# Optimization experiments

Measured on AMD Instinct MI355X. Metric: run time of the kernel, lower is better.

Reference implementation:

```python
import jax, jax.numpy as jnp
import numpy as np

B, N, HS, NH = 32, 256, 768, 32
D = HS // NH  # 24


def setup_inputs() -> dict:
    key = jax.random.key(0)
    ks = jax.random.split(key, 20)
    s = 0.02
    inp = {
        "hidden_states": jax.random.normal(ks[0], (B, N, HS), jnp.float32),
        "attention_bias": jax.random.normal(ks[1], (B, NH, N, N), jnp.float32),
        "delta_pos": jax.random.normal(ks[2], (B, N, N, 3), jnp.float32),
        "attention_mask": jnp.ones((B, N), jnp.float32),
        "Wi": jax.random.normal(ks[3], (HS, HS), jnp.float32) * s,
        "bi": jnp.zeros((HS,), jnp.float32),
        "Wq": jax.random.normal(ks[4], (HS, HS), jnp.float32) * s,
        "bq": jnp.zeros((HS,), jnp.float32),
        "Wk": jax.random.normal(ks[5], (HS, HS), jnp.float32) * s,
        "bk": jnp.zeros((HS,), jnp.float32),
        "Wv": jax.random.normal(ks[6], (HS, HS), jnp.float32) * s,
        "bv": jnp.zeros((HS,), jnp.float32),
        "Wf1": jax.random.normal(ks[7], (1, HS), jnp.float32) * s,
        "bf1": jnp.zeros((1,), jnp.float32),
        "Wf2": jax.random.normal(ks[8], (1, HS), jnp.float32) * s,
        "bf2": jnp.zeros((1,), jnp.float32),
        "Wf3": jax.random.normal(ks[9], (1, HS), jnp.float32) * s,
        "bf3": jnp.zeros((1,), jnp.float32),
    }
    return inp


def reference(hidden_states, attention_bias, delta_pos, attention_mask,
              Wi, bi, Wq, bq, Wk, bk, Wv, bv, Wf1, bf1, Wf2, bf2, Wf3, bf3):
    b, n, hs = hidden_states.shape
    nh = NH
    d = hs // nh
    denoise_scaling = d ** (-0.5)
    scale = np.sqrt(denoise_scaling).astype(np.float32)

    # mask: (B,N) -> additive (B,1,1,N)
    neg = ((1.0 - attention_mask) * -100000.0)[:, None, None, :]

    h = jax.nn.gelu(hidden_states @ Wi.T + bi, approximate=False)
    q = (h @ Wq.T + bq).reshape(b, n, nh, d).transpose(0, 2, 1, 3) * scale
    k = (h @ Wk.T + bk).reshape(b, n, nh, d).transpose(0, 2, 1, 3) * scale
    v = (h @ Wv.T + bv).reshape(b, n, nh, d).transpose(0, 2, 1, 3)

    scores = jnp.einsum('bhid,bhjd->bhij', q, k) + attention_bias + neg
    probs = jax.nn.softmax(scores, axis=-1)  # dropout = identity at eval

    # x[b,i,c,h,d] = sum_j probs[b,h,i,j] * delta_pos[b,i,j,c] * v[b,h,j,d]
    x = jnp.einsum('bhij,bijc,bhjd->bichd', probs, delta_pos, v)
    x = x.reshape(b, n, 3, hs)

    f1 = x[:, :, 0, :] @ Wf1.T + bf1  # (B,N,1)
    f2 = x[:, :, 1, :] @ Wf2.T + bf2
    f3 = x[:, :, 2, :] @ Wf3.T + bf3
    return jnp.concatenate([f1, f2, f3], axis=-1).astype(jnp.float32)
```

## Files before the change

### kernel.cpp

```cpp
#include <hip/hip_runtime.h>
#include <hip/hip_fp16.h>

#define B_  32
#define N_  256
#define HS_ 768
#define NH_ 32
#define D_  24
#define M_  (B_*N_)
#define QKVN 2304

typedef unsigned short us8 __attribute__((ext_vector_type(8)));
typedef _Float16 f16x8 __attribute__((ext_vector_type(8)));
typedef float f32x4 __attribute__((ext_vector_type(4)));

__device__ __forceinline__ unsigned short f2h(float x){
  return __half_as_ushort(__float2half(x));
}
__device__ __forceinline__ float h2f(unsigned short u){
  return __half2float(__ushort_as_half(u));
}
__device__ __forceinline__ void gload16(const void* g, void* l){
  __builtin_amdgcn_global_load_lds(
      (const __attribute__((address_space(1))) void*)g,
      (__attribute__((address_space(3))) void*)l, 16, 0, 0);
}

__global__ __launch_bounds__(256) void cvt_kernel(const float* __restrict__ in,
                                                  unsigned short* __restrict__ out, int n4){
  int i = blockIdx.x*256 + threadIdx.x;
  if (i >= n4) return;
  float4 v = ((const float4*)in)[i];
  ushort4 o;
  o.x = f2h(v.x); o.y = f2h(v.y); o.z = f2h(v.z); o.w = f2h(v.w);
  ((ushort4*)out)[i] = o;
}

__global__ __launch_bounds__(256) void gemm128_kernel(
    const unsigned short* __restrict__ A, const unsigned short* __restrict__ W,
    const float* __restrict__ b0, const float* __restrict__ b1, const float* __restrict__ b2,
    unsigned short* __restrict__ C, int M, int N, int K, int dogelu)
{
  __shared__ unsigned short As[128*64];
  __shared__ unsigned short Bs[128*64];
  int gswz = blockIdx.x;
  int chunkg = gridDim.x >> 3;
  int bid = (gswz & 7)*chunkg + (gswz >> 3);
  int tid = threadIdx.x;
  int nT = N >> 7;
  int tm = bid / nT;
  int tn = bid - tm*nT;
  int which = (tn << 7) / 768;
  const float* bp = (which == 0) ? b0 : (which == 1) ? b1 : b2;
  bp -= which * 768;
  int wave = tid >> 6, lane = tid & 63;
  int wm = (wave >> 1) << 6;
  int wn = (wave & 1) << 6;
  int fr = lane & 15;
  int g  = lane >> 4;

  size_t aoff[4], woff[4];
  int ldsb[4];
#pragma unroll
  for (int s4 = 0; s4 < 4; s4++){
    int ob = s4*4096 + tid*16;
    int r  = ob >> 7;
    int p  = (ob >> 4) & 7;
    int l  = p ^ (r & 7);
    aoff[s4] = ((size_t)(tm*128 + r)*K)*2 + l*16;
    woff[s4] = ((size_t)(tn*128 + r)*K)*2 + l*16;
    ldsb[s4] = s4*4096 + wave*1024;
  }
  const char* Ab = (const char*)A;
  const char* Wb = (const char*)W;
  char* AsB = (char*)As;
  char* BsB = (char*)Bs;

  f32x4 acc[4][4];
#pragma unroll
  for (int m = 0; m < 4; m++)
#pragma unroll
    for (int n = 0; n < 4; n++) acc[m][n] = (f32x4){0.f,0.f,0.f,0.f};

  for (int k0 = 0; k0 < K; k0 += 64){
    size_t kb = (size_t)k0*2;
#pragma unroll
    for (int s4 = 0; s4 < 4; s4++) gload16(Ab + aoff[s4] + kb, AsB + ldsb[s4]);
#pragma unroll
    for (int s4 = 0; s4 < 4; s4++) gload16(Wb + woff[s4] + kb, BsB + ldsb[s4]);
    __syncthreads();

    f16x8 af[4], bf[4];
#pragma unroll
    for (int m = 0; m < 4; m++){
      int row = wm + m*16 + fr;
      af[m] = __builtin_bit_cast(f16x8, *(const us8*)(AsB + row*128 + ((g ^ (row & 7))*16)));
    }
#pragma unroll
    for (int n = 0; n < 4; n++){
      int row = wn + n*16 + fr;
      bf[n] = __builtin_bit_cast(f16x8, *(const us8*)(BsB + row*128 + ((g ^ (row & 7))*16)));
    }
#pragma unroll
    for (int m = 0; m < 4; m++)
#pragma unroll
      for (int n = 0; n < 4; n++)
        acc[m][n] = __builtin_amdgcn_mfma_f32_16x16x32_f16(af[m], bf[n], acc[m][n], 0, 0, 0);

#pragma unroll
    for (int m = 0; m < 4; m++){
      int row = wm + m*16 + fr;
      af[m] = __builtin_bit_cast(f16x8, *(const us8*)(AsB + row*128 + (((g+4) ^ (row & 7))*16)));
    }
#pragma unroll
    for (int n = 0; n < 4; n++){
      int row = wn + n*16 + fr;
      bf[n] = __builtin_bit_cast(f16x8, *(const us8*)(BsB + row*128 + (((g+4) ^ (row & 7))*16)));
    }
#pragma unroll
    for (int m = 0; m < 4; m++)
#pragma unroll
      for (int n = 0; n < 4; n++)
        acc[m][n] = __builtin_amdgcn_mfma_f32_16x16x32_f16(af[m], bf[n], acc[m][n], 0, 0, 0);
    __syncthreads();
  }

#pragma unroll
  for (int n = 0; n < 4; n++){
    int col = tn*128 + wn + n*16 + fr;
    float bv = bp[col];
#pragma unroll
    for (int m = 0; m < 4; m++){
      int row = tm*128 + wm + m*16 + g*4;
#pragma unroll
      for (int q = 0; q < 4; q++){
        float v = acc[m][n][q] + bv;
        if (dogelu) v = 0.5f*v*(1.0f + erff(v*0.70710678118654752f));
        C[(size_t)(row + q)*N + col] = f2h(v);
      }
    }
  }
}

__global__ __launch_bounds__(256) void prep_kernel(
    const unsigned short* __restrict__ qkv, const float* __restrict__ mask,
    const float* __restrict__ Wf1, const float* __restrict__ Wf2, const float* __restrict__ Wf3,
    float* __restrict__ uarr,
    float* __restrict__ negv)
{
  int bh = blockIdx.x;
  int h = bh & 31, b = bh >> 5;
  int j = threadIdx.x;
  const unsigned short* vr = qkv + (size_t)(b*N_ + j)*QKVN + 1536 + h*D_;
  us8 v0 = *(const us8*)(vr);
  us8 v1 = *(const us8*)(vr + 8);
  us8 v2 = *(const us8*)(vr + 16);
  const float* w1 = Wf1 + h*D_;
  const float* w2 = Wf2 + h*D_;
  const float* w3 = Wf3 + h*D_;
  float u0 = 0.f, u1 = 0.f, u2 = 0.f;
#pragma unroll
  for (int e = 0; e < 8; e++){
    float va = h2f(v0[e]), vb2 = h2f(v1[e]), vc = h2f(v2[e]);
    u0 += va*w1[e] + vb2*w1[8+e] + vc*w1[16+e];
    u1 += va*w2[e] + vb2*w2[8+e] + vc*w2[16+e];
    u2 += va*w3[e] + vb2*w3[8+e] + vc*w3[16+e];
  }
  float* ub = uarr + (size_t)bh*3*N_;
  ub[j] = u0; ub[N_ + j] = u1; ub[2*N_ + j] = u2;
  if (h == 0) negv[b*N_ + j] = (1.0f - mask[b*N_ + j]) * -100000.0f;
}

#define SCALE 0.20412414523193154f
#define INVSCALE 4.898979485566356f
#define M0 16.0f
#define BUFSZ 32768
__global__ __launch_bounds__(256, 2) void attn_kernel(
    const unsigned short* __restrict__ qkv,
    const float* __restrict__ bias,
    const float* __restrict__ uarr, const float* __restrict__ negv,
    const float* __restrict__ dp,
    const float* __restrict__ bf1, const float* __restrict__ bf2, const float* __restrict__ bf3,
    float* __restrict__ out)
{
  int gswz = blockIdx.x;
  int lin = (gswz & 7)*64 + (gswz >> 3);
  int b = lin >> 4, chunk = lin & 15;
  int i0 = chunk*16;
  int t = threadIdx.x;
  int wave = t >> 6, lane = t & 63;
  int ch = wave, fr = lane & 15, g = lane >> 4;

  __shared__ __align__(16) char smem[72192];
  char* zp     = smem + 65536;
  float* negsF = (float*)(smem + 69632);
  float* redv  = (float*)(smem + 70656);
  float4* redvE= (float4*)(smem + 71168);

  int bsrc[4];
#pragma unroll
  for (int r = 0; r < 4; r++){
    int a = r*4096 + t*16;
    int row = a >> 10;
    int pc = (a >> 4) & 63;
    int lc = pc ^ (row & 7);
    bsrc[r] = row*1024 + lc*16;
  }
  const char* bb0 = (const char*)bias + (((size_t)(b*32)*256 + i0)*256)*4;
  const char* kq0 = (const char*)(qkv + (size_t)(b*N_ + t)*QKVN + 768);
  const char* ub0 = (const char*)(uarr + (size_t)(b*32)*768);
  const char* uqsrc0;
  int uqstep;
  if (t < 192){ uqsrc0 = ub0 + t*16; uqstep = 3072; }
  else if (t < 240){
    int rr = (t-192)/3, cc = (t-192)%3;
    uqsrc0 = (const char*)(qkv + (size_t)(b*N_ + i0 + rr)*QKVN) + cc*16;
    uqstep = 48;
  } else { uqsrc0 = ub0; uqstep = 3072; }

  #define ISSUE(hh, nx) do { \
    const char* _bB = bb0 + (size_t)(hh)*262144; \
    _Pragma("unroll") \
    for (int _r = 0; _r < 4; _r++) gload16(_bB + bsrc[_r], (nx) + _r*4096 + wave*1024); \
    const char* _kB = kq0 + (hh)*48; \
    _Pragma("unroll") \
    for (int _c = 0; _c < 3; _c++) gload16(_kB + _c*16, (nx) + 16384 + _c*4096 + wave*1024); \
    gload16(uqsrc0 + (size_t)(hh)*uqstep, (nx) + 28672 + wave*1024); \
  } while(0)

  ISSUE(0, smem);
  float4 dpre[12];
  {
    const float* dpb = dp + (size_t)(b*N_ + i0 + fr)*768;
#pragma unroll
    for (int jt = 0; jt < 4; jt++){
      const float4* q4 = (const float4*)(dpb + (ch*64 + jt*16 + g*4)*3);
      dpre[jt*3+0] = q4[0]; dpre[jt*3+1] = q4[1]; dpre[jt*3+2] = q4[2];
    }
  }
  *(us8*)(zp + t*16) = (us8){0,0,0,0,0,0,0,0};
  negsF[t] = negv[b*N_ + t];
  asm volatile("s_waitcnt lgkmcnt(0)" ::: "memory");

  f32x4 G[4][3];
#pragma unroll
  for (int jt = 0; jt < 4; jt++)
#pragma unroll
    for (int c = 0; c < 3; c++) G[jt][c] = (f32x4){0.f,0.f,0.f,0.f};

  int swz = (fr & 7) << 4;

#pragma unroll 1
  for (int h = 0; h < 32; h++){
    int par = h & 1;
    char* bufb = smem + par*BUFSZ;
    char* nxb  = smem + (par^1)*BUFSZ;
    if (h < 31){
      ISSUE(h+1, nxb);
      asm volatile("s_waitcnt vmcnt(8)" ::: "memory");
    } else {
      asm volatile("s_waitcnt vmcnt(0)" ::: "memory");
    }
    __builtin_amdgcn_s_barrier();

    const char* qa = (g < 3) ? (bufb + 28672 + 3072 + fr*48 + g*16) : (zp + fr*16);
    f16x8 qf = __builtin_bit_cast(f16x8, *(const us8*)qa);

    float rowsum = 0.f;
    f32x4 tt[4][3];
#pragma unroll
    for (int jt = 0; jt < 4; jt++){
      int j0 = ch*64 + jt*16 + g*4;
      float4 bv = *(const float4*)(bufb + fr*1024 + ((j0*4) ^ swz));
      float4 nv = *(const float4*)&negsF[j0];
      f32x4 cin;
      cin[0] = (bv.x + nv.x)*INVSCALE;
      cin[1] = (bv.y + nv.y)*INVSCALE;
      cin[2] = (bv.z + nv.z)*INVSCALE;
      cin[3] = (bv.w + nv.w)*INVSCALE;
      int krow = ch*64 + jt*16 + fr;
      const char* ka = (g < 3) ? (bufb + 16384 + g*4096 + krow*16) : (zp + krow*16);
      f16x8 kf = __builtin_bit_cast(f16x8, *(const us8*)ka);
      f32x4 sv = __builtin_amdgcn_mfma_f32_16x16x32_f16(kf, qf, cin, 0, 0, 0);
      f32x4 p;
      p[0] = __expf(fmaf(sv[0], SCALE, -M0));
      p[1] = __expf(fmaf(sv[1], SCALE, -M0));
      p[2] = __expf(fmaf(sv[2], SCALE, -M0));
      p[3] = __expf(fmaf(sv[3], SCALE, -M0));
      rowsum += p[0] + p[1] + p[2] + p[3];
      const char* ub = bufb + 28672;
#pragma unroll
      for (int c = 0; c < 3; c++){
        f32x4 uv = __builtin_bit_cast(f32x4, *(const float4*)(ub + c*1024 + j0*4));
        tt[jt][c] = p * uv;
      }
    }
    rowsum += __shfl_xor(rowsum, 16);
    rowsum += __shfl_xor(rowsum, 32);
    if (lane < 16) redv[(par*16 + fr)*4 + ch] = rowsum;
    asm volatile("s_waitcnt lgkmcnt(0)" ::: "memory");
    __builtin_amdgcn_s_barrier();
    float4 rv = *(const float4*)&redv[(par*16 + fr)*4];
    float rs = 1.0f / (rv.x + rv.y + rv.z + rv.w);
#pragma unroll
    for (int jt = 0; jt < 4; jt++)
#pragma unroll
      for (int c = 0; c < 3; c++){
        G[jt][c][0] = fmaf(rs, tt[jt][c][0], G[jt][c][0]);
        G[jt][c][1] = fmaf(rs, tt[jt][c][1], G[jt][c][1]);
        G[jt][c][2] = fmaf(rs, tt[jt][c][2], G[jt][c][2]);
        G[jt][c][3] = fmaf(rs, tt[jt][c][3], G[jt][c][3]);
      }
  }
  #undef ISSUE

  float a0 = 0.f, a1 = 0.f, a2 = 0.f;
#pragma unroll
  for (int jt = 0; jt < 4; jt++){
    float4 d0 = dpre[jt*3], d1 = dpre[jt*3+1], d2 = dpre[jt*3+2];
    a0 += G[jt][0][0]*d0.x + G[jt][0][1]*d0.w + G[jt][0][2]*d1.z + G[jt][0][3]*d2.y;
    a1 += G[jt][1][0]*d0.y + G[jt][1][1]*d1.x + G[jt][1][2]*d1.w + G[jt][1][3]*d2.z;
    a2 += G[jt][2][0]*d0.z + G[jt][2][1]*d1.y + G[jt][2][2]*d2.x + G[jt][2][3]*d2.w;
  }
  a0 += __shfl_xor(a0, 16); a0 += __shfl_xor(a0, 32);
  a1 += __shfl_xor(a1, 16); a1 += __shfl_xor(a1, 32);
  a2 += __shfl_xor(a2, 16); a2 += __shfl_xor(a2, 32);
  if (lane < 16) redvE[fr*4 + ch] = make_float4(a0, a1, a2, 0.f);
  asm volatile("s_waitcnt lgkmcnt(0)" ::: "memory");
  __builtin_amdgcn_s_barrier();
  if (t < 16){
    float4 e0 = redvE[t*4+0], e1 = redvE[t*4+1], e2 = redvE[t*4+2], e3 = redvE[t*4+3];
    float* op = out + (size_t)(b*N_ + i0 + t)*3;
    op[0] = e0.x + e1.x + e2.x + e3.x + bf1[0];
    op[1] = e0.y + e1.y + e2.y + e3.y + bf2[0];
    op[2] = e0.z + e1.z + e2.z + e3.z + bf3[0];
  }
}

extern "C" void kernel_launch(void* const* d_in, const int* in_sizes, int n_in,
                              void* d_out, int out_size, void* d_ws, size_t ws_size,
                              hipStream_t stream)
{
  const float* X    = (const float*)d_in[0];
  const float* bias = (const float*)d_in[1];
  const float* dp   = (const float*)d_in[2];
  const float* mask = (const float*)d_in[3];
  const float* Wi   = (const float*)d_in[4];
  const float* bi   = (const float*)d_in[5];
  const float* Wq   = (const float*)d_in[6];
  const float* bq   = (const float*)d_in[7];
  const float* Wk   = (const float*)d_in[8];
  const float* bk   = (const float*)d_in[9];
  const float* Wv   = (const float*)d_in[10];
  const float* bv   = (const float*)d_in[11];
  const float* Wf1  = (const float*)d_in[12];
  const float* bf1  = (const float*)d_in[13];
  const float* Wf2  = (const float*)d_in[14];
  const float* bf2  = (const float*)d_in[15];
  const float* Wf3  = (const float*)d_in[16];
  const float* bf3  = (const float*)d_in[17];
  float* out = (float*)d_out;

  unsigned short* xb   = (unsigned short*)d_ws;
  unsigned short* wib  = xb   + (size_t)M_*HS_;
  unsigned short* wqb  = wib  + (size_t)HS_*HS_;
  unsigned short* wkb  = wqb  + (size_t)HS_*HS_;
  unsigned short* wvb  = wkb  + (size_t)HS_*HS_;
  unsigned short* hb   = wvb  + (size_t)HS_*HS_;
  unsigned short* qkvb = hb   + (size_t)M_*HS_;
  float* uarr  = (float*)(qkvb + (size_t)M_*QKVN);
  float* negv  = uarr + (size_t)B_*NH_*3*N_;

  {
    int n4 = M_*HS_/4;
    cvt_kernel<<<n4/256, 256, 0, stream>>>(X, xb, n4);
    int w4 = HS_*HS_/4;
    cvt_kernel<<<w4/256, 256, 0, stream>>>(Wi, wib, w4);
    cvt_kernel<<<w4/256, 256, 0, stream>>>(Wq, wqb, w4);
    cvt_kernel<<<w4/256, 256, 0, stream>>>(Wk, wkb, w4);
    cvt_kernel<<<w4/256, 256, 0, stream>>>(Wv, wvb, w4);
  }

  gemm128_kernel<<<(M_/128)*(HS_/128), 256, 0, stream>>>(xb, wib, bi, bi, bi, hb, M_, HS_, HS_, 1);
  gemm128_kernel<<<(M_/128)*(QKVN/128), 256, 0, stream>>>(hb, wqb, bq, bk, bv, qkvb, M_, QKVN, HS_, 0);

  prep_kernel<<<B_*NH_, 256, 0, stream>>>(qkvb, mask, Wf1, Wf2, Wf3, uarr, negv);

  attn_kernel<<<B_*16, 256, 0, stream>>>(qkvb, bias, uarr, negv, dp,
                                         bf1, bf2, bf3, out);
}
```

Baseline: 181.4 us.

## Deepen bias prefetch to four LDS slots and load K/Q directly into registers

Restructures the attention kernel's per-head pipeline. Bias tiles now go through a 4-slot LDS ring prefetched three heads ahead, while u values use a separate double buffer. K and Q fragments are loaded straight from global memory into ping-ponged registers one head ahead instead of staging them in LDS. The mask values are kept in registers and the delta_pos loads are moved to after the loop to free registers. The aim is to hide more of the bias streaming latency and cut LDS traffic, at the cost of more LDS (75 KB, which still allows 2 blocks per CU) and more in-flight registers.

```diff
diff --git a/kernel.cpp b/kernel.cpp
--- a/kernel.cpp
+++ b/kernel.cpp
@@ -173,7 +173,6 @@
 #define SCALE 0.20412414523193154f
 #define INVSCALE 4.898979485566356f
 #define M0 16.0f
-#define BUFSZ 32768
 __global__ __launch_bounds__(256, 2) void attn_kernel(
     const unsigned short* __restrict__ qkv,
     const float* __restrict__ bias,
@@ -190,11 +189,9 @@
   int wave = t >> 6, lane = t & 63;
   int ch = wave, fr = lane & 15, g = lane >> 4;
 
-  __shared__ __align__(16) char smem[72192];
-  char* zp     = smem + 65536;
-  float* negsF = (float*)(smem + 69632);
-  float* redv  = (float*)(smem + 70656);
-  float4* redvE= (float4*)(smem + 71168);
+  __shared__ __align__(16) char smem[75264];
+  float*  redv  = (float*)(smem + 73728);
+  float4* redvE = (float4*)(smem + 74240);
 
   int bsrc[4];
 #pragma unroll
@@ -206,40 +203,47 @@
     bsrc[r] = row*1024 + lc*16;
   }
   const char* bb0 = (const char*)bias + (((size_t)(b*32)*256 + i0)*256)*4;
-  const char* kq0 = (const char*)(qkv + (size_t)(b*N_ + t)*QKVN + 768);
   const char* ub0 = (const char*)(uarr + (size_t)(b*32)*768);
-  const char* uqsrc0;
-  int uqstep;
-  if (t < 192){ uqsrc0 = ub0 + t*16; uqstep = 3072; }
-  else if (t < 240){
-    int rr = (t-192)/3, cc = (t-192)%3;
-    uqsrc0 = (const char*)(qkv + (size_t)(b*N_ + i0 + rr)*QKVN) + cc*16;
-    uqstep = 48;
-  } else { uqsrc0 = ub0; uqstep = 3072; }
-
-  #define ISSUE(hh, nx) do { \
-    const char* _bB = bb0 + (size_t)(hh)*262144; \
+  int uoff = (t*16 <= 3056) ? t*16 : 3056;
+  const char* kqB = (const char*)qkv;
+  size_t krow[4];
+#pragma unroll
+  for (int jt = 0; jt < 4; jt++)
+    krow[jt] = ((size_t)(b*N_ + ch*64 + jt*16 + fr))*4608 + 1536 + g*16;
+  size_t qrow = ((size_t)(b*N_ + i0 + fr))*4608 + g*16;
+
+  #define ISSUE_BIAS(hh, slot) do { \
+    const char* _s = bb0 + (size_t)(hh)*262144; \
+    char* _d = smem + (slot)*16384; \
     _Pragma("unroll") \
-    for (int _r = 0; _r < 4; _r++) gload16(_bB + bsrc[_r], (nx) + _r*4096 + wave*1024); \
-    const char* _kB = kq0 + (hh)*48; \
+    for (int _r = 0; _r < 4; _r++) gload16(_s + bsrc[_r], _d + _r*4096 + wave*1024); \
+  } while(0)
+  #define ISSUE_U(hh, par) \
+    gload16(ub0 + (size_t)(hh)*3072 + uoff, smem + 65536 + (par)*4096 + wave*1024)
+  #define ISSUE_KQ(hh, kn, qn) do { \
     _Pragma("unroll") \
-    for (int _c = 0; _c < 3; _c++) gload16(_kB + _c*16, (nx) + 16384 + _c*4096 + wave*1024); \
-    gload16(uqsrc0 + (size_t)(hh)*uqstep, (nx) + 28672 + wave*1024); \
+    for (int _jt = 0; _jt < 4; _jt++) \
+      kn[_jt] = __builtin_bit_cast(f16x8, *(const us8*)(kqB + krow[_jt] + (hh)*48)); \
+    qn = __builtin_bit_cast(f16x8, *(const us8*)(kqB + qrow + (hh)*48)); \
   } while(0)
 
-  ISSUE(0, smem);
-  float4 dpre[12];
-  {
-    const float* dpb = dp + (size_t)(b*N_ + i0 + fr)*768;
-#pragma unroll
-    for (int jt = 0; jt < 4; jt++){
-      const float4* q4 = (const float4*)(dpb + (ch*64 + jt*16 + g*4)*3);
-      dpre[jt*3+0] = q4[0]; dpre[jt*3+1] = q4[1]; dpre[jt*3+2] = q4[2];
-    }
-  }
-  *(us8*)(zp + t*16) = (us8){0,0,0,0,0,0,0,0};
-  negsF[t] = negv[b*N_ + t];
-  asm volatile("s_waitcnt lgkmcnt(0)" ::: "memory");
+  float4 nv[4];
+#pragma unroll
+  for (int jt = 0; jt < 4; jt++)
+    nv[jt] = *(const float4*)(negv + b*N_ + ch*64 + jt*16 + g*4);
+
+  f16x8 kA[4], kB[4], qA, qB;
+  f16x8 zero8 = __builtin_bit_cast(f16x8, (us8){0,0,0,0,0,0,0,0});
+
+  ISSUE_BIAS(0, 0);
+  ISSUE_U(0, 0);
+  ISSUE_KQ(0, kA, qA);
+  __builtin_amdgcn_sched_barrier(0);
+  ISSUE_BIAS(1, 1);
+  ISSUE_BIAS(2, 2);
+  __builtin_amdgcn_sched_barrier(0);
+  asm volatile("s_waitcnt vmcnt(8)" ::: "memory");
+  __builtin_amdgcn_s_barrier();
 
   f32x4 G[4][3];
 #pragma unroll
@@ -249,48 +253,43 @@
 
   int swz = (fr & 7) << 4;
 
-#pragma unroll 1
-  for (int h = 0; h < 32; h++){
+  auto body = [&](int h, f16x8 (&kc)[4], f16x8 &qc, f16x8 (&kn)[4], f16x8 &qn)
+      __attribute__((always_inline)) {
+    int hu = (h + 1) & 31;
+    ISSUE_U(hu, (h + 1) & 1);
+    ISSUE_KQ(hu, kn, qn);
+    __builtin_amdgcn_sched_barrier(0);
+    ISSUE_BIAS((h + 3) & 31, (h + 3) & 3);
+    __builtin_amdgcn_sched_barrier(0);
+    asm volatile("s_waitcnt vmcnt(14)" ::: "memory");
+    __builtin_amdgcn_s_barrier();
+
+    const char* bslot = smem + (h & 3)*16384;
+    const char* ubuf  = smem + 65536 + (h & 1)*4096;
+    f16x8 qf = (g < 3) ? qc : zero8;
     int par = h & 1;
-    char* bufb = smem + par*BUFSZ;
-    char* nxb  = smem + (par^1)*BUFSZ;
-    if (h < 31){
-      ISSUE(h+1, nxb);
-      asm volatile("s_waitcnt vmcnt(8)" ::: "memory");
-    } else {
-      asm volatile("s_waitcnt vmcnt(0)" ::: "memory");
-    }
-    __builtin_amdgcn_s_barrier();
-
-    const char* qa = (g < 3) ? (bufb + 28672 + 3072 + fr*48 + g*16) : (zp + fr*16);
-    f16x8 qf = __builtin_bit_cast(f16x8, *(const us8*)qa);
 
     float rowsum = 0.f;
     f32x4 tt[4][3];
 #pragma unroll
     for (int jt = 0; jt < 4; jt++){
       int j0 = ch*64 + jt*16 + g*4;
-      float4 bv = *(const float4*)(bufb + fr*1024 + ((j0*4) ^ swz));
-      float4 nv = *(const float4*)&negsF[j0];
+      float4 bv = *(const float4*)(bslot + fr*1024 + ((j0*4) ^ swz));
       f32x4 cin;
-      cin[0] = (bv.x + nv.x)*INVSCALE;
-      cin[1] = (bv.y + nv.y)*INVSCALE;
-      cin[2] = (bv.z + nv.z)*INVSCALE;
-      cin[3] = (bv.w + nv.w)*INVSCALE;
-      int krow = ch*64 + jt*16 + fr;
-      const char* ka = (g < 3) ? (bufb + 16384 + g*4096 + krow*16) : (zp + krow*16);
-      f16x8 kf = __builtin_bit_cast(f16x8, *(const us8*)ka);
-      f32x4 sv = __builtin_amdgcn_mfma_f32_16x16x32_f16(kf, qf, cin, 0, 0, 0);
+      cin[0] = (bv.x + nv[jt].x)*INVSCALE;
+      cin[1] = (bv.y + nv[jt].y)*INVSCALE;
+      cin[2] = (bv.z + nv[jt].z)*INVSCALE;
+      cin[3] = (bv.w + nv[jt].w)*INVSCALE;
+      f32x4 sv = __builtin_amdgcn_mfma_f32_16x16x32_f16(kc[jt], qf, cin, 0, 0, 0);
       f32x4 p;
       p[0] = __expf(fmaf(sv[0], SCALE, -M0));
       p[1] = __expf(fmaf(sv[1], SCALE, -M0));
       p[2] = __expf(fmaf(sv[2], SCALE, -M0));
       p[3] = __expf(fmaf(sv[3], SCALE, -M0));
       rowsum += p[0] + p[1] + p[2] + p[3];
-      const char* ub = bufb + 28672;
 #pragma unroll
       for (int c = 0; c < 3; c++){
-        f32x4 uv = __builtin_bit_cast(f32x4, *(const float4*)(ub + c*1024 + j0*4));
+        f32x4 uv = __builtin_bit_cast(f32x4, *(const float4*)(ubuf + c*1024 + j0*4));
         tt[jt][c] = p * uv;
       }
     }
@@ -310,16 +309,29 @@
         G[jt][c][2] = fmaf(rs, tt[jt][c][2], G[jt][c][2]);
         G[jt][c][3] = fmaf(rs, tt[jt][c][3], G[jt][c][3]);
       }
-  }
-  #undef ISSUE
+  };
+
+#pragma unroll 1
+  for (int hh = 0; hh < 16; hh++){
+    body(2*hh,     kA, qA, kB, qB);
+    body(2*hh + 1, kB, qB, kA, qA);
+  }
+  asm volatile("s_waitcnt vmcnt(0)" ::: "memory");
+  #undef ISSUE_BIAS
+  #undef ISSUE_U
+  #undef ISSUE_KQ
 
   float a0 = 0.f, a1 = 0.f, a2 = 0.f;
-#pragma unroll
-  for (int jt = 0; jt < 4; jt++){
-    float4 d0 = dpre[jt*3], d1 = dpre[jt*3+1], d2 = dpre[jt*3+2];
-    a0 += G[jt][0][0]*d0.x + G[jt][0][1]*d0.w + G[jt][0][2]*d1.z + G[jt][0][3]*d2.y;
-    a1 += G[jt][1][0]*d0.y + G[jt][1][1]*d1.x + G[jt][1][2]*d1.w + G[jt][1][3]*d2.z;
-    a2 += G[jt][2][0]*d0.z + G[jt][2][1]*d1.y + G[jt][2][2]*d2.x + G[jt][2][3]*d2.w;
+  {
+    const float* dpb = dp + (size_t)(b*N_ + i0 + fr)*768;
+#pragma unroll
+    for (int jt = 0; jt < 4; jt++){
+      const float4* q4 = (const float4*)(dpb + (ch*64 + jt*16 + g*4)*3);
+      float4 d0 = q4[0], d1 = q4[1], d2 = q4[2];
+      a0 += G[jt][0][0]*d0.x + G[jt][0][1]*d0.w + G[jt][0][2]*d1.z + G[jt][0][3]*d2.y;
+      a1 += G[jt][1][0]*d0.y + G[jt][1][1]*d1.x + G[jt][1][2]*d1.w + G[jt][1][3]*d2.z;
+      a2 += G[jt][2][0]*d0.z + G[jt][2][1]*d1.y + G[jt][2][2]*d2.x + G[jt][2][3]*d2.w;
+    }
   }
   a0 += __shfl_xor(a0, 16); a0 += __shfl_xor(a0, 32);
   a1 += __shfl_xor(a1, 16); a1 += __shfl_xor(a1, 32);
```

New measurement: 213.3 us. 1.18x slower.

## Split attention over key halves with partial sums and a separate reduction kernel

Applied to the files above, without the earlier changes.

The attention kernel now splits the key dimension into two halves, doubling the grid to 1024 blocks with half the shared memory and higher occupancy (launch bounds 4). Each block writes per-head partial row sums and weighted sums to a workspace, and a new final kernel normalises and reduces across heads and halves. The per-key Wf projections are stored as packed fp16, and delta_pos is folded in per head instead of at the end. This trades an extra launch, extra global traffic for partials and slightly lower precision in u for more parallelism and fewer in-block barriers.

```diff
diff --git a/kernel.cpp b/kernel.cpp
--- a/kernel.cpp
+++ b/kernel.cpp
@@ -10,6 +10,7 @@
 #define QKVN 2304
 
 typedef unsigned short us8 __attribute__((ext_vector_type(8)));
+typedef unsigned short us4v __attribute__((ext_vector_type(4)));
 typedef _Float16 f16x8 __attribute__((ext_vector_type(8)));
 typedef float f32x4 __attribute__((ext_vector_type(4)));
 
@@ -23,6 +24,9 @@
   __builtin_amdgcn_global_load_lds(
       (const __attribute__((address_space(1))) void*)g,
       (__attribute__((address_space(3))) void*)l, 16, 0, 0);
+}
+__device__ __forceinline__ void pin4(float4 &v){
+  asm volatile("" : "+v"(v.x), "+v"(v.y), "+v"(v.z), "+v"(v.w));
 }
 
 __global__ __launch_bounds__(256) void cvt_kernel(const float* __restrict__ in,
@@ -144,7 +148,7 @@
 __global__ __launch_bounds__(256) void prep_kernel(
     const unsigned short* __restrict__ qkv, const float* __restrict__ mask,
     const float* __restrict__ Wf1, const float* __restrict__ Wf2, const float* __restrict__ Wf3,
-    float* __restrict__ uarr,
+    unsigned short* __restrict__ u16,
     float* __restrict__ negv)
 {
   int bh = blockIdx.x;
@@ -165,175 +169,178 @@
     u1 += va*w2[e] + vb2*w2[8+e] + vc*w2[16+e];
     u2 += va*w3[e] + vb2*w3[8+e] + vc*w3[16+e];
   }
-  float* ub = uarr + (size_t)bh*3*N_;
-  ub[j] = u0; ub[N_ + j] = u1; ub[2*N_ + j] = u2;
+  us4v o = {f2h(u0), f2h(u1), f2h(u2), 0};
+  *(us4v*)(u16 + ((size_t)bh*N_ + j)*4) = o;
   if (h == 0) negv[b*N_ + j] = (1.0f - mask[b*N_ + j]) * -100000.0f;
 }
 
 #define SCALE 0.20412414523193154f
 #define INVSCALE 4.898979485566356f
 #define M0 16.0f
-#define BUFSZ 32768
-__global__ __launch_bounds__(256, 2) void attn_kernel(
+__global__ __launch_bounds__(256, 4) void attn_kernel(
     const unsigned short* __restrict__ qkv,
     const float* __restrict__ bias,
-    const float* __restrict__ uarr, const float* __restrict__ negv,
+    const unsigned short* __restrict__ u16,
+    const float* __restrict__ negv,
     const float* __restrict__ dp,
-    const float* __restrict__ bf1, const float* __restrict__ bf2, const float* __restrict__ bf3,
-    float* __restrict__ out)
+    float* __restrict__ fpart)
 {
   int gswz = blockIdx.x;
-  int lin = (gswz & 7)*64 + (gswz >> 3);
-  int b = lin >> 4, chunk = lin & 15;
-  int i0 = chunk*16;
+  int lin = (gswz & 7)*128 + (gswz >> 3);
+  int b = lin >> 5, ic = (lin >> 1) & 15, jh = lin & 1;
+  int i0 = ic*16, j00 = jh*128;
   int t = threadIdx.x;
   int wave = t >> 6, lane = t & 63;
   int ch = wave, fr = lane & 15, g = lane >> 4;
 
-  __shared__ __align__(16) char smem[72192];
-  char* zp     = smem + 65536;
-  float* negsF = (float*)(smem + 69632);
-  float* redv  = (float*)(smem + 70656);
-  float4* redvE= (float4*)(smem + 71168);
-
-  int bsrc[4];
-#pragma unroll
-  for (int r = 0; r < 4; r++){
-    int a = r*4096 + t*16;
-    int row = a >> 10;
-    int pc = (a >> 4) & 63;
+  __shared__ __align__(16) char smem[35840];
+  char* zp = smem + 32768;
+  char* scratch = smem + 33792;
+
+  int bsrc[2];
+#pragma unroll
+  for (int k = 0; k < 2; k++){
+    int a = k*4096 + t*16;
+    int row = a >> 9;
+    int pc = (a >> 4) & 31;
     int lc = pc ^ (row & 7);
-    bsrc[r] = row*1024 + lc*16;
-  }
-  const char* bb0 = (const char*)bias + (((size_t)(b*32)*256 + i0)*256)*4;
-  const char* kq0 = (const char*)(qkv + (size_t)(b*N_ + t)*QKVN + 768);
-  const char* ub0 = (const char*)(uarr + (size_t)(b*32)*768);
-  const char* uqsrc0;
-  int uqstep;
-  if (t < 192){ uqsrc0 = ub0 + t*16; uqstep = 3072; }
-  else if (t < 240){
-    int rr = (t-192)/3, cc = (t-192)%3;
-    uqsrc0 = (const char*)(qkv + (size_t)(b*N_ + i0 + rr)*QKVN) + cc*16;
-    uqstep = 48;
-  } else { uqsrc0 = ub0; uqstep = 3072; }
-
-  #define ISSUE(hh, nx) do { \
-    const char* _bB = bb0 + (size_t)(hh)*262144; \
-    _Pragma("unroll") \
-    for (int _r = 0; _r < 4; _r++) gload16(_bB + bsrc[_r], (nx) + _r*4096 + wave*1024); \
-    const char* _kB = kq0 + (hh)*48; \
-    _Pragma("unroll") \
-    for (int _c = 0; _c < 3; _c++) gload16(_kB + _c*16, (nx) + 16384 + _c*4096 + wave*1024); \
-    gload16(uqsrc0 + (size_t)(hh)*uqstep, (nx) + 28672 + wave*1024); \
+    bsrc[k] = row*1024 + lc*16;
+  }
+  const char* bb0 = (const char*)bias
+      + ((size_t)(b*NH_)*65536 + (size_t)i0*256 + j00)*4;
+
+  const char* sbase[2]; int sstep[2];
+#pragma unroll
+  for (int k = 0; k < 2; k++){
+    int G = k*256 + t;
+    if (G < 384){
+      int c = G >> 7, r = G & 127;
+      sbase[k] = (const char*)qkv + ((size_t)(b*N_ + j00 + r)*4608 + 1536 + c*16);
+      sstep[k] = 48;
+    } else if (G < 432){
+      int x = G - 384; int i = x/3; int c = x - i*3;
+      sbase[k] = (const char*)qkv + ((size_t)(b*N_ + i0 + i)*4608 + c*16);
+      sstep[k] = 48;
+    } else {
+      int kk = (G < 496) ? (G - 432) : 63;
+      sbase[k] = (const char*)u16 + ((size_t)(b*NH_)*2048 + jh*1024 + kk*16);
+      sstep[k] = 2048;
+    }
+  }
+
+  #define ISSUE(hh) do { \
+    int _par = (hh) & 1; \
+    const char* _bp = bb0 + (size_t)(hh)*262144; \
+    gload16(_bp + bsrc[0], smem + _par*8192 + wave*1024); \
+    gload16(_bp + bsrc[1], smem + _par*8192 + 4096 + wave*1024); \
+    gload16(sbase[0] + (size_t)(hh)*sstep[0], smem + 16384 + _par*8192 + wave*1024); \
+    gload16(sbase[1] + (size_t)(hh)*sstep[1], smem + 16384 + _par*8192 + 4096 + wave*1024); \
   } while(0)
 
-  ISSUE(0, smem);
-  float4 dpre[12];
+  float4 nv[2]; float4 dpre[6];
   {
+    const float* nb = negv + b*N_ + j00;
+#pragma unroll
+    for (int jt = 0; jt < 2; jt++)
+      nv[jt] = *(const float4*)(nb + ch*32 + jt*16 + g*4);
     const float* dpb = dp + (size_t)(b*N_ + i0 + fr)*768;
 #pragma unroll
-    for (int jt = 0; jt < 4; jt++){
-      const float4* q4 = (const float4*)(dpb + (ch*64 + jt*16 + g*4)*3);
-      dpre[jt*3+0] = q4[0]; dpre[jt*3+1] = q4[1]; dpre[jt*3+2] = q4[2];
-    }
-  }
-  *(us8*)(zp + t*16) = (us8){0,0,0,0,0,0,0,0};
-  negsF[t] = negv[b*N_ + t];
+    for (int jt = 0; jt < 2; jt++){
+      const float4* dq = (const float4*)(dpb + (size_t)(j00 + ch*32 + jt*16 + g*4)*3);
+      dpre[jt*3+0] = dq[0]; dpre[jt*3+1] = dq[1]; dpre[jt*3+2] = dq[2];
+    }
+  }
+  asm volatile("s_waitcnt vmcnt(0)" ::: "memory");
+  pin4(nv[0]); pin4(nv[1]);
+#pragma unroll
+  for (int k = 0; k < 6; k++) pin4(dpre[k]);
+
+  ISSUE(0);
+  gload16(negv + b*N_, scratch);
+  if (t < 128) *(us8*)(zp + t*16) = (us8){0,0,0,0,0,0,0,0};
   asm volatile("s_waitcnt lgkmcnt(0)" ::: "memory");
 
-  f32x4 G[4][3];
-#pragma unroll
-  for (int jt = 0; jt < 4; jt++)
-#pragma unroll
-    for (int c = 0; c < 3; c++) G[jt][c] = (f32x4){0.f,0.f,0.f,0.f};
-
   int swz = (fr & 7) << 4;
+  float4* fp4 = (float4*)fpart;
+  size_t fbase = (((size_t)(b*16 + ic)*2 + jh)*32)*64 + ch*16 + fr;
 
 #pragma unroll 1
   for (int h = 0; h < 32; h++){
-    int par = h & 1;
-    char* bufb = smem + par*BUFSZ;
-    char* nxb  = smem + (par^1)*BUFSZ;
-    if (h < 31){
-      ISSUE(h+1, nxb);
-      asm volatile("s_waitcnt vmcnt(8)" ::: "memory");
-    } else {
-      asm volatile("s_waitcnt vmcnt(0)" ::: "memory");
-    }
+    asm volatile("s_waitcnt vmcnt(1)" ::: "memory");
     __builtin_amdgcn_s_barrier();
-
-    const char* qa = (g < 3) ? (bufb + 28672 + 3072 + fr*48 + g*16) : (zp + fr*16);
+    if (h < 31) ISSUE(h+1);
+
+    const char* bslot = smem + (h & 1)*8192;
+    const char* sslot = smem + 16384 + (h & 1)*8192;
+
+    const char* qa = (g < 3) ? (sslot + 6144 + fr*48 + g*16) : (zp + fr*16);
     f16x8 qf = __builtin_bit_cast(f16x8, *(const us8*)qa);
 
-    float rowsum = 0.f;
-    f32x4 tt[4][3];
-#pragma unroll
-    for (int jt = 0; jt < 4; jt++){
-      int j0 = ch*64 + jt*16 + g*4;
-      float4 bv = *(const float4*)(bufb + fr*1024 + ((j0*4) ^ swz));
-      float4 nv = *(const float4*)&negsF[j0];
+    float S = 0.f, a0 = 0.f, a1 = 0.f, a2 = 0.f;
+#pragma unroll
+    for (int jt = 0; jt < 2; jt++){
+      int j0l = ch*32 + jt*16 + g*4;
+      float4 bv = *(const float4*)(bslot + fr*512 + ((j0l*4) ^ swz));
       f32x4 cin;
-      cin[0] = (bv.x + nv.x)*INVSCALE;
-      cin[1] = (bv.y + nv.y)*INVSCALE;
-      cin[2] = (bv.z + nv.z)*INVSCALE;
-      cin[3] = (bv.w + nv.w)*INVSCALE;
-      int krow = ch*64 + jt*16 + fr;
-      const char* ka = (g < 3) ? (bufb + 16384 + g*4096 + krow*16) : (zp + krow*16);
+      cin[0] = (bv.x + nv[jt].x)*INVSCALE;
+      cin[1] = (bv.y + nv[jt].y)*INVSCALE;
+      cin[2] = (bv.z + nv[jt].z)*INVSCALE;
+      cin[3] = (bv.w + nv[jt].w)*INVSCALE;
+      int krow = ch*32 + jt*16 + fr;
+      const char* ka = (g < 3) ? (sslot + g*2048 + krow*16) : (zp + krow*16);
       f16x8 kf = __builtin_bit_cast(f16x8, *(const us8*)ka);
       f32x4 sv = __builtin_amdgcn_mfma_f32_16x16x32_f16(kf, qf, cin, 0, 0, 0);
-      f32x4 p;
-      p[0] = __expf(fmaf(sv[0], SCALE, -M0));
-      p[1] = __expf(fmaf(sv[1], SCALE, -M0));
-      p[2] = __expf(fmaf(sv[2], SCALE, -M0));
-      p[3] = __expf(fmaf(sv[3], SCALE, -M0));
-      rowsum += p[0] + p[1] + p[2] + p[3];
-      const char* ub = bufb + 28672;
-#pragma unroll
-      for (int c = 0; c < 3; c++){
-        f32x4 uv = __builtin_bit_cast(f32x4, *(const float4*)(ub + c*1024 + j0*4));
-        tt[jt][c] = p * uv;
+      float p0 = __expf(fmaf(sv[0], SCALE, -M0));
+      float p1 = __expf(fmaf(sv[1], SCALE, -M0));
+      float p2 = __expf(fmaf(sv[2], SCALE, -M0));
+      float p3 = __expf(fmaf(sv[3], SCALE, -M0));
+      S += p0 + p1 + p2 + p3;
+      us8 ua = *(const us8*)(sslot + 6912 + j0l*8);
+      us8 ub = *(const us8*)(sslot + 6912 + j0l*8 + 16);
+      float4 d0 = dpre[jt*3], d1 = dpre[jt*3+1], d2 = dpre[jt*3+2];
+      a0 += p0*h2f(ua[0])*d0.x + p1*h2f(ua[4])*d0.w + p2*h2f(ub[0])*d1.z + p3*h2f(ub[4])*d2.y;
+      a1 += p0*h2f(ua[1])*d0.y + p1*h2f(ua[5])*d1.x + p2*h2f(ub[1])*d1.w + p3*h2f(ub[5])*d2.z;
+      a2 += p0*h2f(ua[2])*d0.z + p1*h2f(ua[6])*d1.y + p2*h2f(ub[2])*d2.x + p3*h2f(ub[6])*d2.w;
+    }
+    S  += __shfl_xor(S, 16);  S  += __shfl_xor(S, 32);
+    a0 += __shfl_xor(a0, 16); a0 += __shfl_xor(a0, 32);
+    a1 += __shfl_xor(a1, 16); a1 += __shfl_xor(a1, 32);
+    a2 += __shfl_xor(a2, 16); a2 += __shfl_xor(a2, 32);
+    if (lane < 16)
+      fp4[fbase + (size_t)h*64] = make_float4(S, a0, a1, a2);
+  }
+  asm volatile("s_waitcnt vmcnt(0)" ::: "memory");
+  #undef ISSUE
+}
+
+__global__ __launch_bounds__(256) void final_kernel(const float* __restrict__ fpart,
+    const float* __restrict__ bf1, const float* __restrict__ bf2, const float* __restrict__ bf3,
+    float* __restrict__ out)
+{
+  int idx = blockIdx.x*256 + threadIdx.x;
+  int b = idx >> 8, i = idx & 255;
+  int ic = i >> 4, ii = i & 15;
+  const float4* fp4 = (const float4*)fpart;
+  size_t base = ((size_t)(b*16 + ic)*2)*2048 + ii;
+  float acc0 = 0.f, acc1 = 0.f, acc2 = 0.f;
+#pragma unroll 4
+  for (int h = 0; h < 32; h++){
+    float S = 0.f, A0 = 0.f, A1 = 0.f, A2 = 0.f;
+#pragma unroll
+    for (int jh = 0; jh < 2; jh++){
+#pragma unroll
+      for (int ch = 0; ch < 4; ch++){
+        float4 v = fp4[base + (size_t)jh*2048 + (size_t)h*64 + ch*16];
+        S += v.x; A0 += v.y; A1 += v.z; A2 += v.w;
       }
     }
-    rowsum += __shfl_xor(rowsum, 16);
-    rowsum += __shfl_xor(rowsum, 32);
-    if (lane < 16) redv[(par*16 + fr)*4 + ch] = rowsum;
-    asm volatile("s_waitcnt lgkmcnt(0)" ::: "memory");
-    __builtin_amdgcn_s_barrier();
-    float4 rv = *(const float4*)&redv[(par*16 + fr)*4];
-    float rs = 1.0f / (rv.x + rv.y + rv.z + rv.w);
-#pragma unroll
-    for (int jt = 0; jt < 4; jt++)
-#pragma unroll
-      for (int c = 0; c < 3; c++){
-        G[jt][c][0] = fmaf(rs, tt[jt][c][0], G[jt][c][0]);
-        G[jt][c][1] = fmaf(rs, tt[jt][c][1], G[jt][c][1]);
-        G[jt][c][2] = fmaf(rs, tt[jt][c][2], G[jt][c][2]);
-        G[jt][c][3] = fmaf(rs, tt[jt][c][3], G[jt][c][3]);
-      }
-  }
-  #undef ISSUE
-
-  float a0 = 0.f, a1 = 0.f, a2 = 0.f;
-#pragma unroll
-  for (int jt = 0; jt < 4; jt++){
-    float4 d0 = dpre[jt*3], d1 = dpre[jt*3+1], d2 = dpre[jt*3+2];
-    a0 += G[jt][0][0]*d0.x + G[jt][0][1]*d0.w + G[jt][0][2]*d1.z + G[jt][0][3]*d2.y;
-    a1 += G[jt][1][0]*d0.y + G[jt][1][1]*d1.x + G[jt][1][2]*d1.w + G[jt][1][3]*d2.z;
-    a2 += G[jt][2][0]*d0.z + G[jt][2][1]*d1.y + G[jt][2][2]*d2.x + G[jt][2][3]*d2.w;
-  }
-  a0 += __shfl_xor(a0, 16); a0 += __shfl_xor(a0, 32);
-  a1 += __shfl_xor(a1, 16); a1 += __shfl_xor(a1, 32);
-  a2 += __shfl_xor(a2, 16); a2 += __shfl_xor(a2, 32);
-  if (lane < 16) redvE[fr*4 + ch] = make_float4(a0, a1, a2, 0.f);
-  asm volatile("s_waitcnt lgkmcnt(0)" ::: "memory");
-  __builtin_amdgcn_s_barrier();
-  if (t < 16){
-    float4 e0 = redvE[t*4+0], e1 = redvE[t*4+1], e2 = redvE[t*4+2], e3 = redvE[t*4+3];
-    float* op = out + (size_t)(b*N_ + i0 + t)*3;
-    op[0] = e0.x + e1.x + e2.x + e3.x + bf1[0];
-    op[1] = e0.y + e1.y + e2.y + e3.y + bf2[0];
-    op[2] = e0.z + e1.z + e2.z + e3.z + bf3[0];
-  }
+    float rs = 1.0f / S;
+    acc0 += A0*rs; acc1 += A1*rs; acc2 += A2*rs;
+  }
+  float* op = out + (size_t)idx*3;
+  op[0] = acc0 + bf1[0];
+  op[1] = acc1 + bf2[0];
+  op[2] = acc2 + bf3[0];
 }
 
 extern "C" void kernel_launch(void* const* d_in, const int* in_sizes, int n_in,
@@ -367,8 +374,9 @@
   unsigned short* wvb  = wkb  + (size_t)HS_*HS_;
   unsigned short* hb   = wvb  + (size_t)HS_*HS_;
   unsigned short* qkvb = hb   + (size_t)M_*HS_;
-  float* uarr  = (float*)(qkvb + (size_t)M_*QKVN);
-  float* negv  = uarr + (size_t)B_*NH_*3*N_;
+  unsigned short* u16a = qkvb + (size_t)M_*QKVN;
+  float* negv  = (float*)(u16a + (size_t)B_*NH_*N_*4);
+  float* fpart = negv + (size_t)B_*N_;
 
   {
     int n4 = M_*HS_/4;
@@ -383,8 +391,9 @@
   gemm128_kernel<<<(M_/128)*(HS_/128), 256, 0, stream>>>(xb, wib, bi, bi, bi, hb, M_, HS_, HS_, 1);
   gemm128_kernel<<<(M_/128)*(QKVN/128), 256, 0, stream>>>(hb, wqb, bq, bk, bv, qkvb, M_, QKVN, HS_, 0);
 
-  prep_kernel<<<B_*NH_, 256, 0, stream>>>(qkvb, mask, Wf1, Wf2, Wf3, uarr, negv);
-
-  attn_kernel<<<B_*16, 256, 0, stream>>>(qkvb, bias, uarr, negv, dp,
-                                         bf1, bf2, bf3, out);
-}
+  prep_kernel<<<B_*NH_, 256, 0, stream>>>(qkvb, mask, Wf1, Wf2, Wf3, u16a, negv);
+
+  attn_kernel<<<B_*16*2, 256, 0, stream>>>(qkvb, bias, u16a, negv, dp, fpart);
+
+  final_kernel<<<(B_*N_)/256, 256, 0, stream>>>(fpart, bf1, bf2, bf3, out);
+}
```

After: 212.2 us. 1.17x slower.
